# Kernel optimization log

Hardware: AMD Instinct MI355X
Metric: run time of the kernel (lower is better)

## Reference

```python
import jax, jax.numpy as jnp
import numpy as np
import math

DIM = 1024
NUM_HEADS = 16
HEAD_DIM = DIM // NUM_HEADS
ROPE_BASE = 10000.0
LN_EPS = 1e-5


def _rope_tables(seq_len):
    inv_freq = 1.0 / (ROPE_BASE ** (jnp.arange(0, HEAD_DIM, 2, dtype=jnp.float32) / HEAD_DIM))
    t = jnp.arange(seq_len, dtype=jnp.float32)
    freqs = t[:, None] * inv_freq[None, :]            # (T, D/2)
    emb = jnp.concatenate([freqs, freqs], axis=-1)    # (T, D)
    return jnp.cos(emb), jnp.sin(emb)


def _rotate_half(x):
    x1 = x[..., ::2]
    x2 = x[..., 1::2]
    return jnp.stack((-x2, x1), axis=-1).reshape(x.shape)


def _heads(y):
    B, T, _ = y.shape
    return y.reshape(B, T, NUM_HEADS, HEAD_DIM).transpose(0, 2, 1, 3)  # (B,H,T,hd)


def _layernorm(x, w, b):
    mu = jnp.mean(x, axis=-1, keepdims=True)
    var = jnp.var(x, axis=-1, keepdims=True)
    return (x - mu) / jnp.sqrt(var + LN_EPS) * w + b


def setup_inputs() -> dict:
    key = jax.random.key(0)
    ks = jax.random.split(key, 16)
    s = 1.0 / math.sqrt(DIM)
    d = {
        "x": jax.random.normal(ks[0], (2, 2048, DIM), jnp.float32),
        "h_a": jax.random.normal(ks[1], (2, 512, DIM), jnp.float32),
        "h_t": jax.random.normal(ks[2], (2, 64, DIM), jnp.float32),
        "p": jax.random.normal(ks[3], (2, 256, DIM), jnp.float32),
    }
    names = ["Wq", "Wks", "Wvs", "Wka", "Wva", "Wkt", "Wvt", "Wo", "Wf"]
    for i, n in enumerate(names):
        d[n] = jax.random.normal(ks[4 + i], (DIM, DIM), jnp.float32) * s
        d["b" + n[1:]] = jnp.zeros((DIM,), jnp.float32)
    d["gating"] = jnp.zeros((1,), jnp.float32)
    d["ln_w"] = jnp.ones((DIM,), jnp.float32)
    d["ln_b"] = jnp.zeros((DIM,), jnp.float32)
    return d


def reference(x, h_a, h_t, p,
              Wq, bq, Wks, bks, Wvs, bvs, Wka, bka, Wva, bva,
              Wkt, bkt, Wvt, bvt, Wo, bo, Wf, bf,
              gating, ln_w, ln_b):
    B, T, D = x.shape
    g = jnp.tanh(gating)[0]
    h_adapter = jnp.concatenate((h_a, p), axis=1)          # (B, Ta+Tp, D)
    cos, sin = _rope_tables(T)                             # (T, hd)

    q = _heads(x @ Wq + bq)
    ks_ = _heads(x @ Wks + bks)
    vs = _heads(x @ Wvs + bvs)
    q = q * cos + _rotate_half(q) * sin
    ks_ = ks_ * cos + _rotate_half(ks_) * sin

    ka = _heads(h_adapter @ Wka + bka)
    va = _heads(h_adapter @ Wva + bva)
    kt = _heads(h_t @ Wkt + bkt)
    vt = _heads(h_t @ Wvt + bvt)

    s_self = jnp.einsum("bhqd,bhkd->bhqk", q, ks_)
    s_adpt = jnp.einsum("bhqd,bhkd->bhqk", q, ka)
    s_task = jnp.einsum("bhqd,bhkd->bhqk", q, kt) * g
    scores = jnp.concatenate([s_self, s_adpt, s_task], axis=-1) / math.sqrt(HEAD_DIM)
    attn = jax.nn.softmax(scores, axis=-1)                 # (B,H,T,S_total)

    v_all = jnp.concatenate([vs, va, vt], axis=2)          # (B,H,S_total,hd)
    out = jnp.einsum("bhqk,bhkd->bhqd", attn, v_all)
    out = out.transpose(0, 2, 1, 3).reshape(B, T, D)
    out = out @ Wo + bo

    res = _layernorm(out + x, ln_w, ln_b)
    res = jax.nn.relu(res @ Wf + bf)
    return res
```

## Files before the change

kernel.cpp:

```cpp
#include <hip/hip_runtime.h>

typedef __attribute__((ext_vector_type(8))) short bf16x8;
typedef __attribute__((ext_vector_type(4))) float f32x4;
typedef __attribute__((ext_vector_type(8))) unsigned short u16x8;
typedef __attribute__((ext_vector_type(4))) unsigned short u16x4;

#define DEV static __device__ __forceinline__

DEV float bf2f(unsigned short u) {
    union { unsigned int i; float f; } x; x.i = ((unsigned int)u) << 16; return x.f;
}
DEV unsigned short f2bf(float f) {
    union { float f; unsigned int i; } x; x.f = f;
    unsigned int r = x.i + 0x7FFFu + ((x.i >> 16) & 1u);
    return (unsigned short)(r >> 16);
}
DEV unsigned int cvt_pk_bf16(float a, float b) {
    unsigned int r;
    asm("v_cvt_pk_bf16_f32 %0, %1, %2" : "=v"(r) : "v"(a), "v"(b));
    return r;
}
DEV float ldany(const void* p, size_t i, bool f32) {
    return f32 ? ((const float*)p)[i] : bf2f(((const unsigned short*)p)[i]);
}
DEV void gload16(const void* g, void* l) {
    __builtin_amdgcn_global_load_lds(
        (const __attribute__((address_space(1))) unsigned int*)g,
        reinterpret_cast<__attribute__((address_space(3))) unsigned int*>(
            reinterpret_cast<uintptr_t>(l)),
        16, 0, 0);
}

struct Tri  { const void* b0; const void* b1; const void* b2; void* o0; void* o1; void* o2; };
struct W7 {
    const void* w0; const void* w1; const void* w2; const void* w3;
    const void* w4; const void* w5; const void* w6;
};
struct FrontArgs {
    const unsigned short* xb;
    const void* ha; const void* pp; const void* ht;
    const void* bq; const void* bks; const void* bvs;
    const void* bka; const void* bva; const void* bkt; const void* bvt;
    void* qb; void* ks; void* vs; void* kx; void* vx;
    const unsigned short* wtp;
    const unsigned short* wte;
};

__global__ __launch_bounds__(256)
void prep(const void* __restrict__ x, unsigned short* __restrict__ xb,
          float2* __restrict__ tab, const unsigned int* __restrict__ wchk,
          int* __restrict__ flag)
{
    const bool dsf = (wchk[0] == 0x3F800000u);
    const int bid = blockIdx.x, tid = threadIdx.x;
    if (bid < 256) {
        if (bid == 0 && tid == 0) flag[0] = dsf ? 1 : 0;
        const int idx = bid * 256 + tid;
        const int m = idx >> 5, d = idx & 31;
        const float a = (float)m * exp2f(-(float)d * 0.41524101186092033f);
        float sn, cs;
        sincosf(a, &sn, &cs);
        tab[idx] = make_float2(cs, sn);
    } else {
        const size_t off = (size_t)(bid - 256) * 2048 + (size_t)tid * 8;
        if (dsf) {
            const float4* xf = (const float4*)((const float*)x + off);
            const float4 f0 = xf[0], f1 = xf[1];
            u16x8 o;
            unsigned int* d = (unsigned int*)&o;
            d[0] = cvt_pk_bf16(f0.x, f0.y);
            d[1] = cvt_pk_bf16(f0.z, f0.w);
            d[2] = cvt_pk_bf16(f1.x, f1.y);
            d[3] = cvt_pk_bf16(f1.z, f1.w);
            *(u16x8*)(xb + off) = o;
        } else {
            *(u16x8*)(xb + off) = *(const u16x8*)((const unsigned short*)x + off);
        }
    }
}

__global__ __launch_bounds__(256)
void transpose_w7(W7 q, unsigned short* __restrict__ dst1, unsigned short* __restrict__ dst2,
                  int nsplit, const int* __restrict__ flagp)
{
    const bool dsf = (*flagp != 0);
    const int z = blockIdx.z;
    const void* W = (z == 0) ? q.w0 : (z == 1) ? q.w1 : (z == 2) ? q.w2 :
                    (z == 3) ? q.w3 : (z == 4) ? q.w4 : (z == 5) ? q.w5 : q.w6;
    unsigned short* out = (z < nsplit) ? dst1 + ((size_t)z << 20)
                                       : dst2 + ((size_t)(z - nsplit) << 20);
    __shared__ unsigned short Ts[64][72];
    const int t = threadIdx.x;
    const int n0 = blockIdx.x * 64, k0 = blockIdx.y * 64;
    const int r = t >> 2, c = (t & 3) << 4;
    if (!dsf) {
        const unsigned short* Wp = (const unsigned short*)W + (size_t)(k0 + r) * 1024 + n0 + c;
        *(u16x8*)&Ts[r][c]     = *(const u16x8*)Wp;
        *(u16x8*)&Ts[r][c + 8] = *(const u16x8*)(Wp + 8);
    } else {
        const float4* Wf4 = (const float4*)((const float*)W + (size_t)(k0 + r) * 1024 + n0 + c);
        float4 f[4];
        #pragma unroll
        for (int j = 0; j < 4; ++j) f[j] = Wf4[j];
        unsigned int* Td = (unsigned int*)&Ts[r][c];
        #pragma unroll
        for (int j = 0; j < 4; ++j) {
            Td[2 * j]     = cvt_pk_bf16(f[j].x, f[j].y);
            Td[2 * j + 1] = cvt_pk_bf16(f[j].z, f[j].w);
        }
    }
    __syncthreads();
    unsigned short tmp[16];
    #pragma unroll
    for (int j = 0; j < 16; ++j) tmp[j] = Ts[c + j][r];
    unsigned short* op = out + (size_t)(n0 + r) * 1024 + k0 + c;
    *(u16x8*)op       = *(const u16x8*)&tmp[0];
    *(u16x8*)(op + 8) = *(const u16x8*)&tmp[8];
}

__global__ __launch_bounds__(256)
void gemm_front(FrontArgs fa, const int* __restrict__ flagp, const float2* __restrict__ rtab)
{
    const int K = 1024, N = 1024;
    const bool dsf = (*flagp != 0);
    __shared__ unsigned short As[2][128 * 64];
    __shared__ unsigned short Bs[2][128 * 64];
    const int tid = threadIdx.x;
    const int bid0 = blockIdx.y * 8 + blockIdx.x;
    const int bid  = (bid0 & 7) * 122 + (bid0 >> 3);
    const int y  = bid >> 3;
    const int n0 = (bid & 7) << 7;

    const void* A; const unsigned short* WT; const void* bias; void* Cv;
    int m0, rpb_in, rpb_o, row_off; bool rope;
    const bool aasync = (y < 96);
    if (aasync) {
        const int z = y >> 5;
        m0 = (y & 31) << 7;
        A = fa.xb; WT = fa.wtp + ((size_t)z << 20);
        bias = (z == 0) ? fa.bq : (z == 1) ? fa.bks : fa.bvs;
        Cv   = (z == 0) ? fa.qb : (z == 1) ? fa.ks  : fa.vs;
        rpb_in = 1 << 30; rpb_o = 0; row_off = 0;
        rope = (z < 2);
    } else {
        const int ey = y - 96;
        const int w = (ey >= 13) ? 1 : 0;
        const int yy = ey - w * 13;
        int s, m0b;
        if (yy < 8)       { s = 0; m0b = yy; }
        else if (yy < 12) { s = 1; m0b = yy - 8; }
        else              { s = 2; m0b = 0; }
        A = (s == 0) ? fa.ha : (s == 1) ? fa.pp : fa.ht;
        rpb_in  = (s == 0) ? 512 : (s == 1) ? 256 : 64;
        row_off = (s == 0) ? 0 : (s == 1) ? 512 : 768;
        WT   = fa.wte + ((size_t)(((s == 2) ? 2 : 0) + w) << 20);
        bias = (w == 0) ? ((s == 2) ? fa.bkt : fa.bka) : ((s == 2) ? fa.bvt : fa.bva);
        Cv   = (w == 0) ? fa.kx : fa.vx;
        m0 = m0b << 7; rpb_o = 832; rope = false;
    }

    const int lane = tid & 63, wv = tid >> 6;
    const int l3 = lane >> 3, c8 = lane & 7;
    const int swz = (c8 ^ l3) << 3;

    const unsigned short* Bsrc[4];
    #pragma unroll
    for (int j = 0; j < 4; ++j)
        Bsrc[j] = WT + (size_t)(n0 + (wv << 5) + (j << 3) + l3) * K + swz;
    const unsigned short* Asrc[4];
    #pragma unroll
    for (int j = 0; j < 4; ++j)
        Asrc[j] = fa.xb + (size_t)(m0 + (wv << 5) + (j << 3) + l3) * K + swz;

    const int ar = tid >> 1, ch = (tid & 1) << 5, ah = ar & 7, cb = (tid & 1) << 2;
    const size_t arow = (size_t)(m0 + ar) * K + ch;

    const int wm = (wv >> 1) << 6, wn = (wv & 1) << 6;
    const int il = lane & 15, quad = lane >> 4;
    const int h = il & 7;
    const int c0 = ((quad ^ h) << 3);
    int aoff[4], boff[4];
    #pragma unroll
    for (int mi = 0; mi < 4; ++mi) aoff[mi] = (wm + mi * 16 + il) * 64;
    #pragma unroll
    for (int nj = 0; nj < 4; ++nj) boff[nj] = (wn + nj * 16 + il) * 64;

    f32x4 acc[4][4];
    #pragma unroll
    for (int mi = 0; mi < 4; ++mi)
        #pragma unroll
        for (int nj = 0; nj < 4; ++nj) acc[mi][nj] = (f32x4){0.f, 0.f, 0.f, 0.f};

    u16x8 av[4];
    auto loadA = [&](int kq) {
        if (!dsf) {
            const unsigned short* Ag = (const unsigned short*)A + arow + kq;
            #pragma unroll
            for (int j = 0; j < 4; ++j) av[j] = *(const u16x8*)(Ag + 8 * j);
        } else {
            const float4* Af4 = (const float4*)((const float*)A + arow + kq);
            float4 f[8];
            #pragma unroll
            for (int j = 0; j < 8; ++j) f[j] = Af4[j];
            #pragma unroll
            for (int j = 0; j < 4; ++j) {
                unsigned int* d = (unsigned int*)&av[j];
                d[0] = cvt_pk_bf16(f[2 * j].x, f[2 * j].y);
                d[1] = cvt_pk_bf16(f[2 * j].z, f[2 * j].w);
                d[2] = cvt_pk_bf16(f[2 * j + 1].x, f[2 * j + 1].y);
                d[3] = cvt_pk_bf16(f[2 * j + 1].z, f[2 * j + 1].w);
            }
        }
    };
    auto writeA = [&](int buf) {
        #pragma unroll
        for (int j = 0; j < 4; ++j)
            *(u16x8*)&As[buf][ar * 64 + (((cb + j) ^ ah) << 3)] = av[j];
    };
    auto stageB = [&](int buf, int k0) {
        #pragma unroll
        for (int j = 0; j < 4; ++j)
            gload16(Bsrc[j] + k0, &Bs[buf][((wv << 2) + j) << 9]);
    };
    auto stageA = [&](int buf, int k0) {
        #pragma unroll
        for (int j = 0; j < 4; ++j)
            gload16(Asrc[j] + k0, &As[buf][((wv << 2) + j) << 9]);
    };

    if (aasync) {
        stageB(0, 0); stageA(0, 0);
    } else {
        loadA(0); stageB(0, 0); writeA(0); loadA(64);
    }
    __syncthreads();

    for (int k0 = 0; k0 < K; k0 += 64) {
        const int cur = (k0 >> 6) & 1;
        if (k0 + 64 < K) {
            stageB(cur ^ 1, k0 + 64);
            if (aasync) stageA(cur ^ 1, k0 + 64);
            else { writeA(cur ^ 1); if (k0 + 128 < K) loadA(k0 + 128); }
        }
        #pragma unroll
        for (int kk = 0; kk < 2; ++kk) {
            const int cc = c0 ^ (kk << 5);
            bf16x8 af[4], bfr[4];
            #pragma unroll
            for (int mi = 0; mi < 4; ++mi) af[mi] = *(const bf16x8*)&As[cur][aoff[mi] + cc];
            #pragma unroll
            for (int nj = 0; nj < 4; ++nj) bfr[nj] = *(const bf16x8*)&Bs[cur][boff[nj] + cc];
            #pragma unroll
            for (int mi = 0; mi < 4; ++mi)
                #pragma unroll
                for (int nj = 0; nj < 4; ++nj)
                    acc[mi][nj] = __builtin_amdgcn_mfma_f32_16x16x32_bf16(
                        af[mi], bfr[nj], acc[mi][nj], 0, 0, 0);
        }
        __syncthreads();
    }

    float bval[4];
    #pragma unroll
    for (int nj = 0; nj < 4; ++nj) bval[nj] = ldany(bias, n0 + wn + nj * 16 + il, dsf);
    #pragma unroll
    for (int mi = 0; mi < 4; ++mi) {
        #pragma unroll
        for (int r = 0; r < 4; ++r) {
            const int m = m0 + wm + mi * 16 + quad * 4 + r;
            const int bidx = m / rpb_in;
            const size_t orow = (size_t)bidx * rpb_o + row_off + (m - bidx * rpb_in);
            #pragma unroll
            for (int nj = 0; nj < 4; ++nj) {
                float v = acc[mi][nj][r] + bval[nj];
                if (rope) {
                    const int dcol = n0 + wn + nj * 16 + il;
                    const float2 cs2 = rtab[((m & 2047) << 5) | (dcol & 31)];
                    const float partner = __shfl_xor(v, 1);
                    v = (il & 1) ? fmaf(v, cs2.x, partner * cs2.y)
                                 : fmaf(v, cs2.x, -partner * cs2.y);
                }
                ((unsigned short*)Cv)[orow * N + n0 + wn + nj * 16 + il] = f2bf(v);
            }
        }
    }
}

template<int OMODE, bool RELU>
__global__ __launch_bounds__(256)
void gemm_mfma(const void* __restrict__ A, const unsigned short* __restrict__ WT,
               Tri t3, const int* __restrict__ flagp)
{
    const int K = 1024, N = 1024;
    const bool dsf = (*flagp != 0);
    __shared__ unsigned short As[2][128 * 64];
    __shared__ unsigned short Bs[2][128 * 64];
    const int tid = threadIdx.x;
    const int bid0 = blockIdx.y * 8 + blockIdx.x;
    const int bid  = (bid0 & 7) * 32 + (bid0 >> 3);
    const int m0 = (bid >> 3) << 7;
    const int n0 = (bid & 7) << 7;
    const void* bias = t3.b0;
    void* Cv = t3.o0;

    const int lane = tid & 63, wv = tid >> 6;
    const int l3 = lane >> 3, c8 = lane & 7;
    const int swz = (c8 ^ l3) << 3;

    const unsigned short* Bsrc[4];
    #pragma unroll
    for (int j = 0; j < 4; ++j)
        Bsrc[j] = WT + (size_t)(n0 + (wv << 5) + (j << 3) + l3) * K + swz;
    const unsigned short* Asrc[4];
    #pragma unroll
    for (int j = 0; j < 4; ++j)
        Asrc[j] = (const unsigned short*)A + (size_t)(m0 + (wv << 5) + (j << 3) + l3) * K + swz;

    const int wm = (wv >> 1) << 6, wn = (wv & 1) << 6;
    const int il = lane & 15, quad = lane >> 4;
    const int h = il & 7;
    const int c0 = ((quad ^ h) << 3);
    int aoff[4], boff[4];
    #pragma unroll
    for (int mi = 0; mi < 4; ++mi) aoff[mi] = (wm + mi * 16 + il) * 64;
    #pragma unroll
    for (int nj = 0; nj < 4; ++nj) boff[nj] = (wn + nj * 16 + il) * 64;

    f32x4 acc[4][4];
    #pragma unroll
    for (int mi = 0; mi < 4; ++mi)
        #pragma unroll
        for (int nj = 0; nj < 4; ++nj) acc[mi][nj] = (f32x4){0.f, 0.f, 0.f, 0.f};

    auto stageB = [&](int buf, int k0) {
        #pragma unroll
        for (int j = 0; j < 4; ++j)
            gload16(Bsrc[j] + k0, &Bs[buf][((wv << 2) + j) << 9]);
    };
    auto stageA = [&](int buf, int k0) {
        #pragma unroll
        for (int j = 0; j < 4; ++j)
            gload16(Asrc[j] + k0, &As[buf][((wv << 2) + j) << 9]);
    };

    stageB(0, 0);
    stageA(0, 0);
    __syncthreads();

    for (int k0 = 0; k0 < K; k0 += 64) {
        const int cur = (k0 >> 6) & 1;
        if (k0 + 64 < K) {
            stageB(cur ^ 1, k0 + 64);
            stageA(cur ^ 1, k0 + 64);
        }
        #pragma unroll
        for (int kk = 0; kk < 2; ++kk) {
            const int cc = c0 ^ (kk << 5);
            bf16x8 af[4], bfr[4];
            #pragma unroll
            for (int mi = 0; mi < 4; ++mi) af[mi] = *(const bf16x8*)&As[cur][aoff[mi] + cc];
            #pragma unroll
            for (int nj = 0; nj < 4; ++nj) bfr[nj] = *(const bf16x8*)&Bs[cur][boff[nj] + cc];
            #pragma unroll
            for (int mi = 0; mi < 4; ++mi)
                #pragma unroll
                for (int nj = 0; nj < 4; ++nj)
                    acc[mi][nj] = __builtin_amdgcn_mfma_f32_16x16x32_bf16(
                        af[mi], bfr[nj], acc[mi][nj], 0, 0, 0);
        }
        __syncthreads();
    }

    float bval[4];
    #pragma unroll
    for (int nj = 0; nj < 4; ++nj) bval[nj] = ldany(bias, n0 + wn + nj * 16 + il, dsf);
    #pragma unroll
    for (int mi = 0; mi < 4; ++mi) {
        #pragma unroll
        for (int r = 0; r < 4; ++r) {
            const size_t orow = (size_t)(m0 + wm + mi * 16 + quad * 4 + r);
            #pragma unroll
            for (int nj = 0; nj < 4; ++nj) {
                float v = acc[mi][nj][r] + bval[nj];
                if (RELU) v = fmaxf(v, 0.0f);
                const size_t idx = orow * N + n0 + wn + nj * 16 + il;
                if (OMODE == 0) ((unsigned short*)Cv)[idx] = f2bf(v);
                else {
                    if (dsf) ((float*)Cv)[idx] = v;
                    else     ((unsigned short*)Cv)[idx] = f2bf(v);
                }
            }
        }
    }
}

__global__ __launch_bounds__(256)
void attn_mfma(const unsigned short* __restrict__ Q, const unsigned short* __restrict__ Ksf,
               const unsigned short* __restrict__ Vsf, const unsigned short* __restrict__ Kx,
               const unsigned short* __restrict__ Vx, const void* __restrict__ gate,
               const int* __restrict__ flagp, unsigned short* __restrict__ AO)
{
    const int T = 2048, TX = 832, D = 1024;
    __shared__ unsigned short Klds[2][64 * 72];
    __shared__ unsigned short Vlds[2][64 * 72];
    __shared__ unsigned short Plds[4][32 * 72];
    const int tid = threadIdx.x;
    const int bh = blockIdx.x;
    const int b = bh >> 4, h = bh & 15;
    const int t0 = blockIdx.y << 7;
    const bool dsf = (*flagp != 0);
    const float g = tanhf(ldany(gate, 0, dsf));

    const int lane = tid & 63, wv = tid >> 6;
    const int il = lane & 15, quad = lane >> 4;
    const int qw = t0 + (wv << 5);

    bf16x8 qf[2][2];
    #pragma unroll
    for (int mi = 0; mi < 2; ++mi) {
        const unsigned short* qp =
            Q + (size_t)(b * T + qw + mi * 16 + il) * D + (h << 6) + quad * 8;
        qf[mi][0] = *(const bf16x8*)qp;
        qf[mi][1] = *(const bf16x8*)(qp + 32);
    }
    bf16x8 ones;
    #pragma unroll
    for (int e = 0; e < 8; ++e) ((unsigned short*)&ones)[e] = 0x3F80;

    const int ksr = tid >> 2, ksd = (tid & 3) << 4;
    const int t16 = tid >> 4, dg = tid & 15;
    const int vwcol = ((((t16 >> 1) ^ (dg & 3)) << 3) | ((t16 & 1) << 2));
    const int vwrow = (dg << 2) * 72 + vwcol;

    f32x4 o[2][4], ol[2];
    #pragma unroll
    for (int mi = 0; mi < 2; ++mi) {
        ol[mi] = (f32x4){0.f, 0.f, 0.f, 0.f};
        #pragma unroll
        for (int dt = 0; dt < 4; ++dt) o[mi][dt] = (f32x4){0.f, 0.f, 0.f, 0.f};
    }

    const unsigned short* kp = Ksf + (size_t)(b * T + ksr) * D + (h << 6) + ksd;
    const unsigned short* vp = Vsf + (size_t)(b * T + t16) * D + (h << 6) + (dg << 2);

    u16x8 kr0, kr1;
    uint2 vm0, vm1, vm2, vm3;
    auto load_kv = [&]() {
        kr0 = *(const u16x8*)kp; kr1 = *(const u16x8*)(kp + 8);
        vm0 = *(const uint2*)vp;
        vm1 = *(const uint2*)(vp + (1 << 14));
        vm2 = *(const uint2*)(vp + (2 << 14));
        vm3 = *(const uint2*)(vp + (3 << 14));
    };
    load_kv();

    #pragma unroll 1
    for (int kt = 0; kt < 45; ++kt) {
        const int cur = kt & 1;
        *(u16x8*)&Klds[cur][ksr * 72 + ksd]     = kr0;
        *(u16x8*)&Klds[cur][ksr * 72 + ksd + 8] = kr1;
        {
            unsigned int p00 = __builtin_amdgcn_perm(vm1.x, vm0.x, 0x05040100);
            unsigned int p01 = __builtin_amdgcn_perm(vm3.x, vm2.x, 0x05040100);
            unsigned int p10 = __builtin_amdgcn_perm(vm1.x, vm0.x, 0x07060302);
            unsigned int p11 = __builtin_amdgcn_perm(vm3.x, vm2.x, 0x07060302);
            unsigned int p20 = __builtin_amdgcn_perm(vm1.y, vm0.y, 0x05040100);
            unsigned int p21 = __builtin_amdgcn_perm(vm3.y, vm2.y, 0x05040100);
            unsigned int p30 = __builtin_amdgcn_perm(vm1.y, vm0.y, 0x07060302);
            unsigned int p31 = __builtin_amdgcn_perm(vm3.y, vm2.y, 0x07060302);
            *(uint2*)&Vlds[cur][vwrow]           = make_uint2(p00, p01);
            *(uint2*)&Vlds[cur][vwrow + 72]      = make_uint2(p10, p11);
            *(uint2*)&Vlds[cur][vwrow + 144]     = make_uint2(p20, p21);
            *(uint2*)&Vlds[cur][vwrow + 216]     = make_uint2(p30, p31);
        }
        __syncthreads();
        if (kt < 44) {
            if (kt == 31) {
                kp = Kx + (size_t)(b * TX + ksr) * D + (h << 6) + ksd;
                vp = Vx + (size_t)(b * TX + t16) * D + (h << 6) + (dg << 2);
            } else {
                kp += (size_t)64 * D; vp += (size_t)64 * D;
            }
            load_kv();
        }

        f32x4 s[2][4];
        #pragma unroll
        for (int mi = 0; mi < 2; ++mi)
            #pragma unroll
            for (int ct = 0; ct < 4; ++ct) s[mi][ct] = (f32x4){0.f, 0.f, 0.f, 0.f};
        #pragma unroll
        for (int ct = 0; ct < 4; ++ct) {
            #pragma unroll
            for (int c = 0; c < 2; ++c) {
                bf16x8 kf = *(const bf16x8*)&Klds[cur][(ct * 16 + il) * 72 + c * 32 + quad * 8];
                #pragma unroll
                for (int mi = 0; mi < 2; ++mi)
                    s[mi][ct] = __builtin_amdgcn_mfma_f32_16x16x32_bf16(
                        qf[mi][c], kf, s[mi][ct], 0, 0, 0);
            }
        }
        const float fc = ((kt == 44) ? g : 1.0f) * 0.18033688011112042f;

        #pragma unroll
        for (int mi = 0; mi < 2; ++mi)
            #pragma unroll
            for (int r = 0; r < 4; ++r) {
                const float e0 = __builtin_amdgcn_exp2f(fmaf(s[mi][0][r], fc, -11.541560327111708f));
                const float e1 = __builtin_amdgcn_exp2f(fmaf(s[mi][1][r], fc, -11.541560327111708f));
                const float e2 = __builtin_amdgcn_exp2f(fmaf(s[mi][2][r], fc, -11.541560327111708f));
                const float e3 = __builtin_amdgcn_exp2f(fmaf(s[mi][3][r], fc, -11.541560327111708f));
                const unsigned int lo = cvt_pk_bf16(e0, e1);
                const unsigned int hi = cvt_pk_bf16(e2, e3);
                *(uint2*)&Plds[wv][(mi * 16 + quad * 4 + r) * 72 + (il << 2)] =
                    make_uint2(lo, hi);
            }

        #pragma unroll
        for (int c = 0; c < 2; ++c) {
            bf16x8 pf[2];
            #pragma unroll
            for (int mi = 0; mi < 2; ++mi)
                pf[mi] = *(const bf16x8*)&Plds[wv][(mi * 16 + il) * 72 + c * 32 + quad * 8];
            #pragma unroll
            for (int mi = 0; mi < 2; ++mi)
                ol[mi] = __builtin_amdgcn_mfma_f32_16x16x32_bf16(pf[mi], ones, ol[mi], 0, 0, 0);
            #pragma unroll
            for (int dt = 0; dt < 4; ++dt) {
                bf16x8 vf = *(const bf16x8*)
                    &Vlds[cur][(dt * 16 + il) * 72 + c * 32 + ((quad ^ (il >> 2)) << 3)];
                #pragma unroll
                for (int mi = 0; mi < 2; ++mi)
                    o[mi][dt] = __builtin_amdgcn_mfma_f32_16x16x32_bf16(
                        pf[mi], vf, o[mi][dt], 0, 0, 0);
            }
        }
    }

    #pragma unroll
    for (int mi = 0; mi < 2; ++mi) {
        float invl[4];
        #pragma unroll
        for (int r = 0; r < 4; ++r) invl[r] = 1.0f / ol[mi][r];
        #pragma unroll
        for (int dt = 0; dt < 4; ++dt)
            #pragma unroll
            for (int r = 0; r < 4; ++r)
                AO[(size_t)(b * T + qw + mi * 16 + quad * 4 + r) * D + (h << 6) + dt * 16 + il] =
                    f2bf(o[mi][dt][r] * invl[r]);
    }
}

__global__ __launch_bounds__(256)
void ln_res(const unsigned short* __restrict__ proj, const void* __restrict__ x,
            const void* __restrict__ w, const void* __restrict__ bb,
            const int* __restrict__ flagp, unsigned short* __restrict__ y)
{
    const int row = blockIdx.x;
    const int tid = threadIdx.x;
    const bool dsf = (*flagp != 0);
    const unsigned short* pr = proj + (size_t)row * 1024;
    const u16x4 p4 = *(const u16x4*)(pr + (tid << 2));
    float v[4];
    if (dsf) {
        const float4 x4 = *(const float4*)((const float*)x + (size_t)row * 1024 + (tid << 2));
        v[0] = bf2f(p4[0]) + x4.x; v[1] = bf2f(p4[1]) + x4.y;
        v[2] = bf2f(p4[2]) + x4.z; v[3] = bf2f(p4[3]) + x4.w;
    } else {
        const u16x4 x4 = *(const u16x4*)((const unsigned short*)x + (size_t)row * 1024 + (tid << 2));
        #pragma unroll
        for (int e = 0; e < 4; ++e) v[e] = bf2f(p4[e]) + bf2f(x4[e]);
    }
    float s1 = v[0] + v[1] + v[2] + v[3];
    float s2 = v[0]*v[0] + v[1]*v[1] + v[2]*v[2] + v[3]*v[3];
    #pragma unroll
    for (int off = 1; off < 64; off <<= 1) {
        s1 += __shfl_xor(s1, off);
        s2 += __shfl_xor(s2, off);
    }
    __shared__ float red1[4], red2[4];
    const int wv = tid >> 6;
    if ((tid & 63) == 0) { red1[wv] = s1; red2[wv] = s2; }
    __syncthreads();
    s1 = red1[0] + red1[1] + red1[2] + red1[3];
    s2 = red2[0] + red2[1] + red2[2] + red2[3];
    const float mu = s1 * (1.0f / 1024.0f);
    const float var = s2 * (1.0f / 1024.0f) - mu * mu;
    const float rstd = rsqrtf(var + 1e-5f);
    float wv4[4], bv4[4];
    if (dsf) {
        const float4 wf = *(const float4*)((const float*)w + (tid << 2));
        const float4 bf4 = *(const float4*)((const float*)bb + (tid << 2));
        wv4[0] = wf.x; wv4[1] = wf.y; wv4[2] = wf.z; wv4[3] = wf.w;
        bv4[0] = bf4.x; bv4[1] = bf4.y; bv4[2] = bf4.z; bv4[3] = bf4.w;
    } else {
        const u16x4 wf = *(const u16x4*)((const unsigned short*)w + (tid << 2));
        const u16x4 bf4 = *(const u16x4*)((const unsigned short*)bb + (tid << 2));
        #pragma unroll
        for (int e = 0; e < 4; ++e) { wv4[e] = bf2f(wf[e]); bv4[e] = bf2f(bf4[e]); }
    }
    u16x4 o4;
    #pragma unroll
    for (int e = 0; e < 4; ++e)
        o4[e] = f2bf((v[e] - mu) * rstd * wv4[e] + bv4[e]);
    *(u16x4*)(y + (size_t)row * 1024 + (tid << 2)) = o4;
}

extern "C" void kernel_launch(void* const* d_in, const int* in_sizes, int n_in,
                              void* d_out, int out_size, void* d_ws, size_t ws_size,
                              hipStream_t stream)
{
    const void* x    = d_in[0];
    const void* h_a  = d_in[1];
    const void* h_t  = d_in[2];
    const void* p    = d_in[3];
    const void* Wq   = d_in[4];
    const void* bq   = d_in[5];
    const void* Wks  = d_in[6];
    const void* bks  = d_in[7];
    const void* Wvs  = d_in[8];
    const void* bvs  = d_in[9];
    const void* Wka  = d_in[10];
    const void* bka  = d_in[11];
    const void* Wva  = d_in[12];
    const void* bva  = d_in[13];
    const void* Wkt  = d_in[14];
    const void* bkt  = d_in[15];
    const void* Wvt  = d_in[16];
    const void* bvt  = d_in[17];
    const void* Wo   = d_in[18];
    const void* bo   = d_in[19];
    const void* Wf   = d_in[20];
    const void* bf_  = d_in[21];
    const void* gating = d_in[22];
    const void* ln_w = d_in[23];
    const void* ln_b = d_in[24];

    char* ws = (char*)d_ws;
    int*            flag = (int*)ws;
    unsigned short* qb   = (unsigned short*)(ws + 256);
    unsigned short* ks   = (unsigned short*)(ws + 8388864);
    unsigned short* vs   = (unsigned short*)(ws + 16777472);
    unsigned short* kx   = (unsigned short*)(ws + 25166080);
    unsigned short* vx   = (unsigned short*)(ws + 28573952);
    unsigned short* ao   = (unsigned short*)(ws + 31981824);
    unsigned short* proj  = ks;
    unsigned short* lnout = vs;
    unsigned short* WT1 = ao;
    unsigned short* WTd = (unsigned short*)d_out;
    unsigned short* xb  = WTd + ((size_t)4 << 20);
    unsigned short* WT3 = kx;
    float2*         rtab = (float2*)(ws + 31981824 + 6291456);

    dim3 blk(256);
    const Tri nul = {};

    prep<<<2304, blk, 0, stream>>>(x, xb, rtab, (const unsigned int*)ln_w, flag);

    {
        W7 w7 = {Wq, Wks, Wvs, Wka, Wva, Wkt, Wvt};
        transpose_w7<<<dim3(16, 16, 7), blk, 0, stream>>>(w7, WT1, WTd, 3, flag);
    }

    {
        FrontArgs fa = {xb, h_a, p, h_t,
                        bq, bks, bvs, bka, bva, bkt, bvt,
                        qb, ks, vs, kx, vx, WT1, WTd};
        gemm_front<<<dim3(8, 122), blk, 0, stream>>>(fa, flag, rtab);
    }

    attn_mfma<<<dim3(32, 16), blk, 0, stream>>>(qb, ks, vs, kx, vx, gating, flag, ao);

    {
        W7 w2 = {Wo, Wf, Wf, Wf, Wf, Wf, Wf};
        transpose_w7<<<dim3(16, 16, 2), blk, 0, stream>>>(w2, WT3, WT3, 2, flag);
    }
    {
        Tri t3 = {bo, nul.b1, nul.b2, proj, nul.o1, nul.o2};
        gemm_mfma<0, false><<<dim3(8, 32), blk, 0, stream>>>(ao, WT3, t3, flag);
    }
    ln_res<<<4096, blk, 0, stream>>>(proj, x, ln_w, ln_b, flag, lnout);
    {
        Tri t3 = {bf_, nul.b1, nul.b2, d_out, nul.o1, nul.o2};
        gemm_mfma<2, true><<<dim3(8, 32), blk, 0, stream>>>(
            lnout, WT3 + ((size_t)1 << 20), t3, flag);
    }
}
```

Before: 354.1 us.

## Single-buffer front GEMM LDS and halve back GEMM M-tile for more blocks

The front QKV/adapter GEMM drops its double-buffered LDS staging and instead loads and syncs each K-slice before computing. This halves its shared memory so more blocks fit per CU, but loads no longer overlap with MFMA work in the same block. The output-projection and FFN GEMMs move from 128x128 to 64x128 tiles with twice the grid, so 512 blocks spread over the CUs instead of 256. The cost is less reuse of B tiles per block.

New measurement: 348.8 us. No clear change (-1.5%).

```diff
diff --git a/kernel.cpp b/kernel.cpp
--- a/kernel.cpp
+++ b/kernel.cpp
@@ -123,8 +123,8 @@
 {
     const int K = 1024, N = 1024;
     const bool dsf = (*flagp != 0);
-    __shared__ unsigned short As[2][128 * 64];
-    __shared__ unsigned short Bs[2][128 * 64];
+    __shared__ unsigned short As[128 * 64];
+    __shared__ unsigned short Bs[128 * 64];
     const int tid = threadIdx.x;
     const int bid0 = blockIdx.y * 8 + blockIdx.x;
     const int bid  = (bid0 & 7) * 122 + (bid0 >> 3);
@@ -212,44 +212,38 @@
             }
         }
     };
-    auto writeA = [&](int buf) {
+    auto writeA = [&]() {
         #pragma unroll
         for (int j = 0; j < 4; ++j)
-            *(u16x8*)&As[buf][ar * 64 + (((cb + j) ^ ah) << 3)] = av[j];
+            *(u16x8*)&As[ar * 64 + (((cb + j) ^ ah) << 3)] = av[j];
     };
-    auto stageB = [&](int buf, int k0) {
+    auto stageB = [&](int k0) {
         #pragma unroll
         for (int j = 0; j < 4; ++j)
-            gload16(Bsrc[j] + k0, &Bs[buf][((wv << 2) + j) << 9]);
+            gload16(Bsrc[j] + k0, &Bs[((wv << 2) + j) << 9]);
     };
-    auto stageA = [&](int buf, int k0) {
+    auto stageA = [&](int k0) {
         #pragma unroll
         for (int j = 0; j < 4; ++j)
-            gload16(Asrc[j] + k0, &As[buf][((wv << 2) + j) << 9]);
+            gload16(Asrc[j] + k0, &As[((wv << 2) + j) << 9]);
     };
 
-    if (aasync) {
-        stageB(0, 0); stageA(0, 0);
-    } else {
-        loadA(0); stageB(0, 0); writeA(0); loadA(64);
-    }
-    __syncthreads();
+    if (!aasync) loadA(0);
 
     for (int k0 = 0; k0 < K; k0 += 64) {
-        const int cur = (k0 >> 6) & 1;
-        if (k0 + 64 < K) {
-            stageB(cur ^ 1, k0 + 64);
-            if (aasync) stageA(cur ^ 1, k0 + 64);
-            else { writeA(cur ^ 1); if (k0 + 128 < K) loadA(k0 + 128); }
-        }
+        if (aasync) stageA(k0);
+        else        writeA();
+        stageB(k0);
+        __syncthreads();
+        if (!aasync && k0 + 64 < K) loadA(k0 + 64);
         #pragma unroll
         for (int kk = 0; kk < 2; ++kk) {
             const int cc = c0 ^ (kk << 5);
             bf16x8 af[4], bfr[4];
             #pragma unroll
-            for (int mi = 0; mi < 4; ++mi) af[mi] = *(const bf16x8*)&As[cur][aoff[mi] + cc];
-            #pragma unroll
-            for (int nj = 0; nj < 4; ++nj) bfr[nj] = *(const bf16x8*)&Bs[cur][boff[nj] + cc];
+            for (int mi = 0; mi < 4; ++mi) af[mi] = *(const bf16x8*)&As[aoff[mi] + cc];
+            #pragma unroll
+            for (int nj = 0; nj < 4; ++nj) bfr[nj] = *(const bf16x8*)&Bs[boff[nj] + cc];
             #pragma unroll
             for (int mi = 0; mi < 4; ++mi)
                 #pragma unroll
@@ -288,17 +282,17 @@
 
 template<int OMODE, bool RELU>
 __global__ __launch_bounds__(256)
-void gemm_mfma(const void* __restrict__ A, const unsigned short* __restrict__ WT,
+void gemm_back(const void* __restrict__ A, const unsigned short* __restrict__ WT,
                Tri t3, const int* __restrict__ flagp)
 {
     const int K = 1024, N = 1024;
     const bool dsf = (*flagp != 0);
-    __shared__ unsigned short As[2][128 * 64];
+    __shared__ unsigned short As[2][64 * 64];
     __shared__ unsigned short Bs[2][128 * 64];
     const int tid = threadIdx.x;
     const int bid0 = blockIdx.y * 8 + blockIdx.x;
-    const int bid  = (bid0 & 7) * 32 + (bid0 >> 3);
-    const int m0 = (bid >> 3) << 7;
+    const int bid  = (bid0 & 7) * 64 + (bid0 >> 3);
+    const int m0 = (bid >> 3) << 6;
     const int n0 = (bid & 7) << 7;
     const void* bias = t3.b0;
     void* Cv = t3.o0;
@@ -311,24 +305,24 @@
     #pragma unroll
     for (int j = 0; j < 4; ++j)
         Bsrc[j] = WT + (size_t)(n0 + (wv << 5) + (j << 3) + l3) * K + swz;
-    const unsigned short* Asrc[4];
-    #pragma unroll
-    for (int j = 0; j < 4; ++j)
-        Asrc[j] = (const unsigned short*)A + (size_t)(m0 + (wv << 5) + (j << 3) + l3) * K + swz;
-
-    const int wm = (wv >> 1) << 6, wn = (wv & 1) << 6;
+    const unsigned short* Asrc[2];
+    #pragma unroll
+    for (int j = 0; j < 2; ++j)
+        Asrc[j] = (const unsigned short*)A + (size_t)(m0 + (wv << 4) + (j << 3) + l3) * K + swz;
+
+    const int wm = (wv >> 1) << 5, wn = (wv & 1) << 6;
     const int il = lane & 15, quad = lane >> 4;
     const int h = il & 7;
     const int c0 = ((quad ^ h) << 3);
-    int aoff[4], boff[4];
-    #pragma unroll
-    for (int mi = 0; mi < 4; ++mi) aoff[mi] = (wm + mi * 16 + il) * 64;
+    int aoff[2], boff[4];
+    #pragma unroll
+    for (int mi = 0; mi < 2; ++mi) aoff[mi] = (wm + mi * 16 + il) * 64;
     #pragma unroll
     for (int nj = 0; nj < 4; ++nj) boff[nj] = (wn + nj * 16 + il) * 64;
 
-    f32x4 acc[4][4];
-    #pragma unroll
-    for (int mi = 0; mi < 4; ++mi)
+    f32x4 acc[2][4];
+    #pragma unroll
+    for (int mi = 0; mi < 2; ++mi)
         #pragma unroll
         for (int nj = 0; nj < 4; ++nj) acc[mi][nj] = (f32x4){0.f, 0.f, 0.f, 0.f};
 
@@ -339,8 +333,8 @@
     };
     auto stageA = [&](int buf, int k0) {
         #pragma unroll
-        for (int j = 0; j < 4; ++j)
-            gload16(Asrc[j] + k0, &As[buf][((wv << 2) + j) << 9]);
+        for (int j = 0; j < 2; ++j)
+            gload16(Asrc[j] + k0, &As[buf][((wv << 1) + j) << 9]);
     };
 
     stageB(0, 0);
@@ -356,13 +350,13 @@
         #pragma unroll
         for (int kk = 0; kk < 2; ++kk) {
             const int cc = c0 ^ (kk << 5);
-            bf16x8 af[4], bfr[4];
-            #pragma unroll
-            for (int mi = 0; mi < 4; ++mi) af[mi] = *(const bf16x8*)&As[cur][aoff[mi] + cc];
+            bf16x8 af[2], bfr[4];
+            #pragma unroll
+            for (int mi = 0; mi < 2; ++mi) af[mi] = *(const bf16x8*)&As[cur][aoff[mi] + cc];
             #pragma unroll
             for (int nj = 0; nj < 4; ++nj) bfr[nj] = *(const bf16x8*)&Bs[cur][boff[nj] + cc];
             #pragma unroll
-            for (int mi = 0; mi < 4; ++mi)
+            for (int mi = 0; mi < 2; ++mi)
                 #pragma unroll
                 for (int nj = 0; nj < 4; ++nj)
                     acc[mi][nj] = __builtin_amdgcn_mfma_f32_16x16x32_bf16(
@@ -375,7 +369,7 @@
     #pragma unroll
     for (int nj = 0; nj < 4; ++nj) bval[nj] = ldany(bias, n0 + wn + nj * 16 + il, dsf);
     #pragma unroll
-    for (int mi = 0; mi < 4; ++mi) {
+    for (int mi = 0; mi < 2; ++mi) {
         #pragma unroll
         for (int r = 0; r < 4; ++r) {
             const size_t orow = (size_t)(m0 + wm + mi * 16 + quad * 4 + r);
@@ -677,12 +671,12 @@
     }
     {
         Tri t3 = {bo, nul.b1, nul.b2, proj, nul.o1, nul.o2};
-        gemm_mfma<0, false><<<dim3(8, 32), blk, 0, stream>>>(ao, WT3, t3, flag);
+        gemm_back<0, false><<<dim3(8, 64), blk, 0, stream>>>(ao, WT3, t3, flag);
     }
     ln_res<<<4096, blk, 0, stream>>>(proj, x, ln_w, ln_b, flag, lnout);
     {
         Tri t3 = {bf_, nul.b1, nul.b2, d_out, nul.o1, nul.o2};
-        gemm_mfma<2, true><<<dim3(8, 32), blk, 0, stream>>>(
+        gemm_back<2, true><<<dim3(8, 64), blk, 0, stream>>>(
             lnout, WT3 + ((size_t)1 << 20), t3, flag);
     }
 }
```
